# Optimization experiments

Hardware: AMD Instinct MI355X
Metric: run time of the kernel (lower is better)

Reference implementation:

```python
import jax, jax.numpy as jnp
import numpy as np
import math

N, E = 50000, 800000
NFEAT, HID, NCLASS = 512, 96, 64
NUM_LAYERS = 8
ALPHA, THETA = 0.1, 0.5


def setup_inputs() -> dict:
    key = jax.random.key(0)
    ks = jax.random.split(key, 8)
    x = jax.random.normal(ks[0], (N, NFEAT), dtype=jnp.float32)
    # dense_to_sparse(adj_t) -> edge_index; weights are discarded by the module,
    # so propagation uses unit edge weights. We generate the edge list directly.
    edge_index = jax.random.randint(ks[1], (2, E), 0, N, dtype=jnp.int32)
    s_in = 1.0 / math.sqrt(NFEAT)
    s_hid = 1.0 / math.sqrt(HID)
    W_in = jax.random.uniform(ks[2], (NFEAT, HID), jnp.float32, -s_in, s_in)
    b_in = jax.random.uniform(ks[3], (HID,), jnp.float32, -s_in, s_in)
    conv_W = jax.random.uniform(ks[4], (NUM_LAYERS, HID, HID), jnp.float32, -s_hid, s_hid)
    W_out = jax.random.uniform(ks[5], (HID, NCLASS), jnp.float32, -s_hid, s_hid)
    b_out = jax.random.uniform(ks[6], (NCLASS,), jnp.float32, -s_hid, s_hid)
    return {"x": x, "edge_index": edge_index, "W_in": W_in, "b_in": b_in,
            "conv_W": conv_W, "W_out": W_out, "b_out": b_out}


def reference(x, edge_index, W_in, b_in, conv_W, W_out, b_out):
    # Eval mode: dropout is identity.
    src, dst = edge_index[0], edge_index[1]
    h = jax.nn.relu(x @ W_in + b_in)          # [N, HID]
    x0 = h
    for layer in range(NUM_LAYERS):
        beta = math.log(THETA / (layer + 1) + 1.0)
        # sparse propagation: out[i] = sum over edges (j -> i) of h[j]
        agg = jax.ops.segment_sum(h[src], dst, num_segments=N)   # [N, HID]
        hc = (1.0 - ALPHA) * agg + ALPHA * x0                    # initial residual
        h = jax.nn.relu((1.0 - beta) * hc + beta * (hc @ conv_W[layer]))
    out = h @ W_out + b_out                   # [N, NCLASS]
    return jax.nn.log_softmax(out, axis=-1)
```

## Files before the change

### kernel.cpp

```cpp
#include <hip/hip_runtime.h>
#include <math.h>

#define N_NODES 50000
#define N_EDGES 800000
#define NFEAT   512
#define HID     96
#define NCLASS  64
#define NUM_LAYERS 8
#define ALPHA   0.1f
#define NSB     49
#define NBB     196

typedef __attribute__((ext_vector_type(8))) short short8;
typedef __attribute__((ext_vector_type(4))) float f32x4;

__device__ __forceinline__ unsigned short f2bf(float f) {
    unsigned int u = __float_as_uint(f);
    unsigned int r = u + 0x7FFF + ((u >> 16) & 1);
    return (unsigned short)(r >> 16);
}
__device__ __forceinline__ float bflo(unsigned int u) { return __uint_as_float(u << 16); }
__device__ __forceinline__ float bfhi(unsigned int u) { return __uint_as_float(u & 0xFFFF0000u); }
__device__ __forceinline__ float bf2f(short s) {
    return __uint_as_float(((unsigned int)(unsigned short)s) << 16);
}

__global__ void hist_kernel(const int* __restrict__ dst, int* __restrict__ deg) {
    int e = blockIdx.x * blockDim.x + threadIdx.x;
    if (e < N_EDGES) atomicAdd(&deg[dst[e]], 1);
}

__global__ void scan1_kernel(const int* __restrict__ deg, int* __restrict__ row_start,
                             int* __restrict__ blk_sum) {
    __shared__ int sd[1024];
    int t = threadIdx.x;
    int i = blockIdx.x * 1024 + t;
    int v = (i < N_NODES) ? ((deg[i] + 3) & ~3) : 0;
    sd[t] = v;
    __syncthreads();
    for (int off = 1; off < 1024; off <<= 1) {
        int tv = (t >= off) ? sd[t - off] : 0;
        __syncthreads();
        sd[t] += tv;
        __syncthreads();
    }
    if (i < N_NODES) row_start[i] = sd[t] - v;
    if (t == 1023) blk_sum[blockIdx.x] = sd[1023];
}

__global__ void scan2_kernel(const int* __restrict__ blk_sum, int* __restrict__ blk_off) {
    if (threadIdx.x == 0) {
        int acc = 0;
        for (int b = 0; b < NSB; b++) { blk_off[b] = acc; acc += blk_sum[b]; }
    }
}

__global__ void scan3_kernel(int* __restrict__ row_start, const int* __restrict__ blk_off) {
    int i = blockIdx.x * 1024 + threadIdx.x;
    if (i < N_NODES) row_start[i] += blk_off[blockIdx.x];
}

__global__ void fill_kernel(const int* __restrict__ src, const int* __restrict__ dst,
                            const int* __restrict__ row_start, int* __restrict__ cursor,
                            int* __restrict__ csr_src) {
    int e = blockIdx.x * blockDim.x + threadIdx.x;
    if (e < N_EDGES) {
        int d = dst[e];
        int pos = row_start[d] + atomicAdd(&cursor[d], 1);
        csr_src[pos] = src[e];
    }
}

__global__ void pad_kernel(const int* __restrict__ deg, const int* __restrict__ row_start,
                           int* __restrict__ csr_src) {
    int n = blockIdx.x * blockDim.x + threadIdx.x;
    if (n < N_NODES) {
        int d = deg[n], pd = (d + 3) & ~3, rs = row_start[n];
        for (int p = d; p < pd; p++) csr_src[rs + p] = N_NODES;
    }
}

__global__ __launch_bounds__(256) void bin_hist2_kernel(
        const int* __restrict__ deg, int* __restrict__ node_rank,
        int* __restrict__ blk_bin_cnt) {
    __shared__ int lh[64];
    int t = threadIdx.x;
    if (t < 64) lh[t] = 0;
    __syncthreads();
    int n = blockIdx.x * 256 + t;
    if (n < N_NODES) {
        int nq = (deg[n] + 3) >> 2; if (nq > 63) nq = 63;
        node_rank[n] = atomicAdd(&lh[nq], 1);
    }
    __syncthreads();
    if (t < 64) blk_bin_cnt[blockIdx.x * 64 + t] = lh[t];
}

__global__ void bin_offsets_kernel(const int* __restrict__ blk_bin_cnt,
                                   int* __restrict__ blk_bin_off,
                                   int* __restrict__ bin_base) {
    __shared__ int tot[64];
    int b = threadIdx.x;
    int acc = 0;
    for (int blk = 0; blk < NBB; blk++) {
        blk_bin_off[blk * 64 + b] = acc;
        acc += blk_bin_cnt[blk * 64 + b];
    }
    tot[b] = acc;
    __syncthreads();
    if (b == 0) {
        int a = 0;
        for (int i = 63; i >= 0; i--) { bin_base[i] = a; a += tot[i]; }
    }
}

__global__ __launch_bounds__(256) void bin_place_kernel(
        const int* __restrict__ deg, const int* __restrict__ node_rank,
        const int* __restrict__ blk_bin_off, const int* __restrict__ bin_base,
        int* __restrict__ perm) {
    int n = blockIdx.x * 256 + threadIdx.x;
    if (n < N_NODES) {
        int nq = (deg[n] + 3) >> 2; if (nq > 63) nq = 63;
        perm[bin_base[nq] + blk_bin_off[blockIdx.x * 64 + nq] + node_rank[n]] = n;
    }
}

__global__ void zero_dummy_kernel(short* __restrict__ h0, short* __restrict__ hb,
                                  short* __restrict__ hc) {
    int t = threadIdx.x;
    if (t < HID) {
        h0[(size_t)N_NODES * HID + t] = 0;
        hb[(size_t)N_NODES * HID + t] = 0;
        hc[(size_t)N_NODES * HID + t] = 0;
    }
}

__global__ void convert_win_kernel(const float* __restrict__ W, short* __restrict__ Wt) {
    int n = blockIdx.x;
    int k = threadIdx.x;
    Wt[(size_t)n * NFEAT + k] = (short)f2bf(W[(size_t)k * HID + n]);
}

__global__ void convert_wout_kernel(const float* __restrict__ W, short* __restrict__ Wt) {
    int n = blockIdx.x;
    int k = threadIdx.x;
    Wt[(size_t)n * HID + k] = (short)f2bf(W[(size_t)k * NCLASS + n]);
}

__global__ void convert_wconv_kernel(const float* __restrict__ W, short* __restrict__ Wc) {
    int n = blockIdx.x;
    int l = blockIdx.y;
    int k = threadIdx.x;
    Wc[(size_t)l * HID * HID + (size_t)n * HID + k] =
        (short)f2bf(W[(size_t)l * HID * HID + (size_t)k * HID + n]);
}

__global__ __launch_bounds__(256) void gemm_in_kernel(
        const float* __restrict__ x, const short* __restrict__ Wt,
        const float* __restrict__ b, short* __restrict__ h0) {
    int tid  = threadIdx.x;
    int wave = tid >> 6, lane = tid & 63;
    int quad = lane >> 4, l16 = lane & 15;
    int row0 = blockIdx.x * 64 + wave * 16;
    int arow = row0 + l16; if (arow >= N_NODES) arow = N_NODES - 1;
    const float* xrow = &x[(size_t)arow * NFEAT];
    const short* wrow = &Wt[(size_t)l16 * NFEAT + quad * 8];

    f32x4 acc[6];
#pragma unroll
    for (int n = 0; n < 6; n++) acc[n] = (f32x4){0.f, 0.f, 0.f, 0.f};

#pragma unroll
    for (int k0 = 0; k0 < NFEAT; k0 += 32) {
        float4 v0 = *(const float4*)&xrow[k0 + quad * 8];
        float4 v1 = *(const float4*)&xrow[k0 + quad * 8 + 4];
        union { short8 s; uint4 u; } af;
        af.u.x = (unsigned)f2bf(v0.x) | ((unsigned)f2bf(v0.y) << 16);
        af.u.y = (unsigned)f2bf(v0.z) | ((unsigned)f2bf(v0.w) << 16);
        af.u.z = (unsigned)f2bf(v1.x) | ((unsigned)f2bf(v1.y) << 16);
        af.u.w = (unsigned)f2bf(v1.z) | ((unsigned)f2bf(v1.w) << 16);
#pragma unroll
        for (int n = 0; n < 6; n++) {
            short8 bfrag = *(const short8*)&wrow[(size_t)n * 16 * NFEAT + k0];
            acc[n] = __builtin_amdgcn_mfma_f32_16x16x32_bf16(af.s, bfrag, acc[n], 0, 0, 0);
        }
    }
#pragma unroll
    for (int n = 0; n < 6; n++) {
        int col = n * 16 + l16;
        float bias = b[col];
#pragma unroll
        for (int r = 0; r < 4; r++) {
            int grow = row0 + quad * 4 + r;
            if (grow < N_NODES) {
                float v = acc[n][r] + bias;
                v = v > 0.f ? v : 0.f;
                h0[(size_t)grow * HID + col] = (short)f2bf(v);
            }
        }
    }
}

__global__ __launch_bounds__(384) void layer_kernel(
        const short* __restrict__ h_in, const short* __restrict__ x0bf,
        const int* __restrict__ row_start, const int* __restrict__ deg,
        const int* __restrict__ csr_src, const int* __restrict__ perm,
        const short* __restrict__ Wc, float beta, short* __restrict__ h_out) {
    __shared__ short As[32][104];
    __shared__ int   snode[32];
    int tid = threadIdx.x;
    int tx = tid % 12;
    int ty = tid / 12;
    int idx = blockIdx.x * 32 + ty;
    bool valid = idx < N_NODES;
    int node = valid ? perm[idx] : (N_NODES - 1);
    if (tx == 0) snode[ty] = valid ? node : -1;

    int s = row_start[node];
    int d = deg[node];
    int nq = (d + 3) >> 2;
    const int4* c4 = (const int4*)(csr_src + s);
    float acc[8];
#pragma unroll
    for (int j = 0; j < 8; j++) acc[j] = 0.f;
    for (int i = 0; i < nq; i++) {
        int4 idxv = c4[i];
        uint4 a0 = *(const uint4*)&h_in[(size_t)idxv.x * HID + tx * 8];
        uint4 a1 = *(const uint4*)&h_in[(size_t)idxv.y * HID + tx * 8];
        uint4 a2 = *(const uint4*)&h_in[(size_t)idxv.z * HID + tx * 8];
        uint4 a3 = *(const uint4*)&h_in[(size_t)idxv.w * HID + tx * 8];
        acc[0] += bflo(a0.x) + bflo(a1.x) + bflo(a2.x) + bflo(a3.x);
        acc[1] += bfhi(a0.x) + bfhi(a1.x) + bfhi(a2.x) + bfhi(a3.x);
        acc[2] += bflo(a0.y) + bflo(a1.y) + bflo(a2.y) + bflo(a3.y);
        acc[3] += bfhi(a0.y) + bfhi(a1.y) + bfhi(a2.y) + bfhi(a3.y);
        acc[4] += bflo(a0.z) + bflo(a1.z) + bflo(a2.z) + bflo(a3.z);
        acc[5] += bfhi(a0.z) + bfhi(a1.z) + bfhi(a2.z) + bfhi(a3.z);
        acc[6] += bflo(a0.w) + bflo(a1.w) + bflo(a2.w) + bflo(a3.w);
        acc[7] += bfhi(a0.w) + bfhi(a1.w) + bfhi(a2.w) + bfhi(a3.w);
    }
    uint4 xq = *(const uint4*)&x0bf[(size_t)node * HID + tx * 8];
    float hc[8];
    hc[0] = (1.f - ALPHA) * acc[0] + ALPHA * bflo(xq.x);
    hc[1] = (1.f - ALPHA) * acc[1] + ALPHA * bfhi(xq.x);
    hc[2] = (1.f - ALPHA) * acc[2] + ALPHA * bflo(xq.y);
    hc[3] = (1.f - ALPHA) * acc[3] + ALPHA * bfhi(xq.y);
    hc[4] = (1.f - ALPHA) * acc[4] + ALPHA * bflo(xq.z);
    hc[5] = (1.f - ALPHA) * acc[5] + ALPHA * bfhi(xq.z);
    hc[6] = (1.f - ALPHA) * acc[6] + ALPHA * bflo(xq.w);
    hc[7] = (1.f - ALPHA) * acc[7] + ALPHA * bfhi(xq.w);
    {
        uint4 pk;
        pk.x = (unsigned)f2bf(hc[0]) | ((unsigned)f2bf(hc[1]) << 16);
        pk.y = (unsigned)f2bf(hc[2]) | ((unsigned)f2bf(hc[3]) << 16);
        pk.z = (unsigned)f2bf(hc[4]) | ((unsigned)f2bf(hc[5]) << 16);
        pk.w = (unsigned)f2bf(hc[6]) | ((unsigned)f2bf(hc[7]) << 16);
        *(uint4*)&As[ty][tx * 8] = pk;
    }
    __syncthreads();

    int wave = tid >> 6, lane = tid & 63;
    int quad = lane >> 4, l16 = lane & 15;
    int rt = wave & 1;
    int ct0 = (wave >> 1) * 2, ct1 = ct0 + 1;

    f32x4 g0 = (f32x4){0.f,0.f,0.f,0.f}, g1 = (f32x4){0.f,0.f,0.f,0.f};
#pragma unroll
    for (int ks = 0; ks < 3; ks++) {
        short8 afrag = *(const short8*)&As[rt * 16 + l16][ks * 32 + quad * 8];
        short8 b0 = *(const short8*)&Wc[(size_t)(ct0 * 16 + l16) * HID + ks * 32 + quad * 8];
        short8 b1 = *(const short8*)&Wc[(size_t)(ct1 * 16 + l16) * HID + ks * 32 + quad * 8];
        g0 = __builtin_amdgcn_mfma_f32_16x16x32_bf16(afrag, b0, g0, 0, 0, 0);
        g1 = __builtin_amdgcn_mfma_f32_16x16x32_bf16(afrag, b1, g1, 0, 0, 0);
    }
    float ob = 1.0f - beta;
#pragma unroll
    for (int r = 0; r < 4; r++) {
        int lrow = rt * 16 + quad * 4 + r;
        int nd = snode[lrow];
        if (nd >= 0) {
            int c0 = ct0 * 16 + l16;
            int c1 = ct1 * 16 + l16;
            float v0 = ob * bf2f(As[lrow][c0]) + beta * g0[r];
            float v1 = ob * bf2f(As[lrow][c1]) + beta * g1[r];
            v0 = v0 > 0.f ? v0 : 0.f;
            v1 = v1 > 0.f ? v1 : 0.f;
            h_out[(size_t)nd * HID + c0] = (short)f2bf(v0);
            h_out[(size_t)nd * HID + c1] = (short)f2bf(v1);
        }
    }
}

__global__ __launch_bounds__(256) void out_kernel(
        const short* __restrict__ h_bf, const short* __restrict__ Wt,
        const float* __restrict__ b, float* __restrict__ out) {
    int tid = threadIdx.x;
    int wave = tid >> 6, lane = tid & 63;
    int quad = lane >> 4, l16 = lane & 15;
    int row0 = blockIdx.x * 64 + wave * 16;

    f32x4 acc[4];
#pragma unroll
    for (int n = 0; n < 4; n++) acc[n] = (f32x4){0.f, 0.f, 0.f, 0.f};

    int arow = row0 + l16; if (arow > N_NODES) arow = N_NODES;
#pragma unroll
    for (int ks = 0; ks < 3; ks++) {
        short8 afrag = *(const short8*)&h_bf[(size_t)arow * HID + ks * 32 + quad * 8];
#pragma unroll
        for (int n = 0; n < 4; n++) {
            short8 bfrag = *(const short8*)&Wt[(size_t)(n * 16 + l16) * HID + ks * 32 + quad * 8];
            acc[n] = __builtin_amdgcn_mfma_f32_16x16x32_bf16(afrag, bfrag, acc[n], 0, 0, 0);
        }
    }
#pragma unroll
    for (int n = 0; n < 4; n++) {
        float bias = b[n * 16 + l16];
#pragma unroll
        for (int r = 0; r < 4; r++) acc[n][r] += bias;
    }
#pragma unroll
    for (int r = 0; r < 4; r++) {
        float m = acc[0][r];
        m = fmaxf(m, acc[1][r]); m = fmaxf(m, acc[2][r]); m = fmaxf(m, acc[3][r]);
#pragma unroll
        for (int off = 1; off < 16; off <<= 1) m = fmaxf(m, __shfl_xor(m, off));
        float s = __expf(acc[0][r] - m) + __expf(acc[1][r] - m)
                + __expf(acc[2][r] - m) + __expf(acc[3][r] - m);
#pragma unroll
        for (int off = 1; off < 16; off <<= 1) s += __shfl_xor(s, off);
        float lse = m + __logf(s);
        int grow = row0 + quad * 4 + r;
        if (grow < N_NODES) {
#pragma unroll
            for (int n = 0; n < 4; n++)
                out[(size_t)grow * NCLASS + n * 16 + l16] = acc[n][r] - lse;
        }
    }
}

extern "C" void kernel_launch(void* const* d_in, const int* in_sizes, int n_in,
                              void* d_out, int out_size, void* d_ws, size_t ws_size,
                              hipStream_t stream) {
    const float* x      = (const float*)d_in[0];
    const int*   ei     = (const int*)d_in[1];
    const int*   srcp   = ei;
    const int*   dstp   = ei + N_EDGES;
    const float* W_in   = (const float*)d_in[2];
    const float* b_in   = (const float*)d_in[3];
    const float* conv_W = (const float*)d_in[4];
    const float* W_out  = (const float*)d_in[5];
    const float* b_out  = (const float*)d_in[6];
    float* out = (float*)d_out;

    short* h0  = (short*)d_ws;
    short* h_b = h0  + (size_t)(N_NODES + 1) * HID;
    short* h_c = h_b + (size_t)(N_NODES + 1) * HID;
    short* Wt_in  = h_c + (size_t)(N_NODES + 1) * HID;
    short* Wt_out = Wt_in + (size_t)HID * NFEAT;
    short* Wc     = Wt_out + (size_t)NCLASS * HID;
    int* deg        = (int*)(Wc + (size_t)NUM_LAYERS * HID * HID);
    int* row_start  = deg + N_NODES;
    int* cursor     = row_start + N_NODES;
    int* blk_sum    = cursor + N_NODES;
    int* blk_off    = blk_sum + 64;
    int* bin_base   = blk_off + 64;
    int* node_rank  = bin_base + 64;
    int* perm       = node_rank + N_NODES;
    int* blk_bin_cnt= perm + N_NODES;
    int* blk_bin_off= blk_bin_cnt + NBB * 64;
    int* csr_src    = blk_bin_off + NBB * 64;

    hipMemsetAsync(deg,    0, N_NODES * sizeof(int), stream);
    hipMemsetAsync(cursor, 0, N_NODES * sizeof(int), stream);
    hist_kernel<<<(N_EDGES + 255) / 256, 256, 0, stream>>>(dstp, deg);
    scan1_kernel<<<NSB, 1024, 0, stream>>>(deg, row_start, blk_sum);
    scan2_kernel<<<1, 64, 0, stream>>>(blk_sum, blk_off);
    scan3_kernel<<<NSB, 1024, 0, stream>>>(row_start, blk_off);
    fill_kernel<<<(N_EDGES + 255) / 256, 256, 0, stream>>>(srcp, dstp, row_start, cursor, csr_src);
    pad_kernel<<<(N_NODES + 255) / 256, 256, 0, stream>>>(deg, row_start, csr_src);
    bin_hist2_kernel<<<NBB, 256, 0, stream>>>(deg, node_rank, blk_bin_cnt);
    bin_offsets_kernel<<<1, 64, 0, stream>>>(blk_bin_cnt, blk_bin_off, bin_base);
    bin_place_kernel<<<NBB, 256, 0, stream>>>(deg, node_rank, blk_bin_off, bin_base, perm);

    convert_win_kernel<<<HID, NFEAT, 0, stream>>>(W_in, Wt_in);
    convert_wout_kernel<<<NCLASS, HID, 0, stream>>>(W_out, Wt_out);
    convert_wconv_kernel<<<dim3(HID, NUM_LAYERS), HID, 0, stream>>>(conv_W, Wc);
    gemm_in_kernel<<<(N_NODES + 63) / 64, 256, 0, stream>>>(x, Wt_in, b_in, h0);
    zero_dummy_kernel<<<1, 128, 0, stream>>>(h0, h_b, h_c);

    short* cur = h0;
    short* nxt = h_b;
    for (int l = 0; l < NUM_LAYERS; l++) {
        float beta = logf(0.5f / (float)(l + 1) + 1.0f);
        layer_kernel<<<(N_NODES + 31) / 32, 384, 0, stream>>>(
            cur, h0, row_start, deg, csr_src, perm, Wc + (size_t)l * HID * HID, beta, nxt);
        cur = nxt;
        nxt = (cur == h_b) ? h_c : h_b;
    }

    out_kernel<<<(N_NODES + 63) / 64, 256, 0, stream>>>(cur, Wt_out, b_out, out);
}
```

Measured before the change: 563.3 us.

## Pad hidden row stride to 128, unroll gather by 8, split input GEMM columns

Hidden-state buffers use a 128-element row stride so each gathered row is 256-byte aligned, aiming to reduce cache lines touched per random neighbor fetch. CSR rows are padded to multiples of 8 and the aggregation loop gathers 8 neighbors per iteration for more memory-level parallelism. The input GEMM is split into two column halves across a second grid dimension, raising parallelism but reading x twice. Padding also raises memory footprint and wasted padded-edge work for low-degree nodes.

```diff
diff --git a/kernel.cpp b/kernel.cpp
--- a/kernel.cpp
+++ b/kernel.cpp
@@ -5,6 +5,7 @@
 #define N_EDGES 800000
 #define NFEAT   512
 #define HID     96
+#define HSTR    128
 #define NCLASS  64
 #define NUM_LAYERS 8
 #define ALPHA   0.1f
@@ -35,7 +36,7 @@
     __shared__ int sd[1024];
     int t = threadIdx.x;
     int i = blockIdx.x * 1024 + t;
-    int v = (i < N_NODES) ? ((deg[i] + 3) & ~3) : 0;
+    int v = (i < N_NODES) ? ((deg[i] + 7) & ~7) : 0;
     sd[t] = v;
     __syncthreads();
     for (int off = 1; off < 1024; off <<= 1) {
@@ -75,7 +76,7 @@
                            int* __restrict__ csr_src) {
     int n = blockIdx.x * blockDim.x + threadIdx.x;
     if (n < N_NODES) {
-        int d = deg[n], pd = (d + 3) & ~3, rs = row_start[n];
+        int d = deg[n], pd = (d + 7) & ~7, rs = row_start[n];
         for (int p = d; p < pd; p++) csr_src[rs + p] = N_NODES;
     }
 }
@@ -89,7 +90,7 @@
     __syncthreads();
     int n = blockIdx.x * 256 + t;
     if (n < N_NODES) {
-        int nq = (deg[n] + 3) >> 2; if (nq > 63) nq = 63;
+        int nq = (deg[n] + 7) >> 3; if (nq > 63) nq = 63;
         node_rank[n] = atomicAdd(&lh[nq], 1);
     }
     __syncthreads();
@@ -120,7 +121,7 @@
         int* __restrict__ perm) {
     int n = blockIdx.x * 256 + threadIdx.x;
     if (n < N_NODES) {
-        int nq = (deg[n] + 3) >> 2; if (nq > 63) nq = 63;
+        int nq = (deg[n] + 7) >> 3; if (nq > 63) nq = 63;
         perm[bin_base[nq] + blk_bin_off[blockIdx.x * 64 + nq] + node_rank[n]] = n;
     }
 }
@@ -128,10 +129,10 @@
 __global__ void zero_dummy_kernel(short* __restrict__ h0, short* __restrict__ hb,
                                   short* __restrict__ hc) {
     int t = threadIdx.x;
-    if (t < HID) {
-        h0[(size_t)N_NODES * HID + t] = 0;
-        hb[(size_t)N_NODES * HID + t] = 0;
-        hc[(size_t)N_NODES * HID + t] = 0;
+    if (t < HSTR) {
+        h0[(size_t)N_NODES * HSTR + t] = 0;
+        hb[(size_t)N_NODES * HSTR + t] = 0;
+        hc[(size_t)N_NODES * HSTR + t] = 0;
     }
 }
 
@@ -162,13 +163,14 @@
     int wave = tid >> 6, lane = tid & 63;
     int quad = lane >> 4, l16 = lane & 15;
     int row0 = blockIdx.x * 64 + wave * 16;
+    int ch   = blockIdx.y;
     int arow = row0 + l16; if (arow >= N_NODES) arow = N_NODES - 1;
     const float* xrow = &x[(size_t)arow * NFEAT];
-    const short* wrow = &Wt[(size_t)l16 * NFEAT + quad * 8];
-
-    f32x4 acc[6];
-#pragma unroll
-    for (int n = 0; n < 6; n++) acc[n] = (f32x4){0.f, 0.f, 0.f, 0.f};
+    const short* wrow = &Wt[(size_t)(ch * 48 + l16) * NFEAT + quad * 8];
+
+    f32x4 acc[3];
+#pragma unroll
+    for (int n = 0; n < 3; n++) acc[n] = (f32x4){0.f, 0.f, 0.f, 0.f};
 
 #pragma unroll
     for (int k0 = 0; k0 < NFEAT; k0 += 32) {
@@ -180,14 +182,14 @@
         af.u.z = (unsigned)f2bf(v1.x) | ((unsigned)f2bf(v1.y) << 16);
         af.u.w = (unsigned)f2bf(v1.z) | ((unsigned)f2bf(v1.w) << 16);
 #pragma unroll
-        for (int n = 0; n < 6; n++) {
+        for (int n = 0; n < 3; n++) {
             short8 bfrag = *(const short8*)&wrow[(size_t)n * 16 * NFEAT + k0];
             acc[n] = __builtin_amdgcn_mfma_f32_16x16x32_bf16(af.s, bfrag, acc[n], 0, 0, 0);
         }
     }
 #pragma unroll
-    for (int n = 0; n < 6; n++) {
-        int col = n * 16 + l16;
+    for (int n = 0; n < 3; n++) {
+        int col = ch * 48 + n * 16 + l16;
         float bias = b[col];
 #pragma unroll
         for (int r = 0; r < 4; r++) {
@@ -195,7 +197,7 @@
             if (grow < N_NODES) {
                 float v = acc[n][r] + bias;
                 v = v > 0.f ? v : 0.f;
-                h0[(size_t)grow * HID + col] = (short)f2bf(v);
+                h0[(size_t)grow * HSTR + col] = (short)f2bf(v);
             }
         }
     }
@@ -218,27 +220,40 @@
 
     int s = row_start[node];
     int d = deg[node];
-    int nq = (d + 3) >> 2;
+    int n8 = (d + 7) >> 3;
     const int4* c4 = (const int4*)(csr_src + s);
     float acc[8];
 #pragma unroll
     for (int j = 0; j < 8; j++) acc[j] = 0.f;
-    for (int i = 0; i < nq; i++) {
-        int4 idxv = c4[i];
-        uint4 a0 = *(const uint4*)&h_in[(size_t)idxv.x * HID + tx * 8];
-        uint4 a1 = *(const uint4*)&h_in[(size_t)idxv.y * HID + tx * 8];
-        uint4 a2 = *(const uint4*)&h_in[(size_t)idxv.z * HID + tx * 8];
-        uint4 a3 = *(const uint4*)&h_in[(size_t)idxv.w * HID + tx * 8];
-        acc[0] += bflo(a0.x) + bflo(a1.x) + bflo(a2.x) + bflo(a3.x);
-        acc[1] += bfhi(a0.x) + bfhi(a1.x) + bfhi(a2.x) + bfhi(a3.x);
-        acc[2] += bflo(a0.y) + bflo(a1.y) + bflo(a2.y) + bflo(a3.y);
-        acc[3] += bfhi(a0.y) + bfhi(a1.y) + bfhi(a2.y) + bfhi(a3.y);
-        acc[4] += bflo(a0.z) + bflo(a1.z) + bflo(a2.z) + bflo(a3.z);
-        acc[5] += bfhi(a0.z) + bfhi(a1.z) + bfhi(a2.z) + bfhi(a3.z);
-        acc[6] += bflo(a0.w) + bflo(a1.w) + bflo(a2.w) + bflo(a3.w);
-        acc[7] += bfhi(a0.w) + bfhi(a1.w) + bfhi(a2.w) + bfhi(a3.w);
-    }
-    uint4 xq = *(const uint4*)&x0bf[(size_t)node * HID + tx * 8];
+    for (int i = 0; i < n8; i++) {
+        int4 ia = c4[2 * i];
+        int4 ib = c4[2 * i + 1];
+        uint4 a0 = *(const uint4*)&h_in[(size_t)ia.x * HSTR + tx * 8];
+        uint4 a1 = *(const uint4*)&h_in[(size_t)ia.y * HSTR + tx * 8];
+        uint4 a2 = *(const uint4*)&h_in[(size_t)ia.z * HSTR + tx * 8];
+        uint4 a3 = *(const uint4*)&h_in[(size_t)ia.w * HSTR + tx * 8];
+        uint4 a4 = *(const uint4*)&h_in[(size_t)ib.x * HSTR + tx * 8];
+        uint4 a5 = *(const uint4*)&h_in[(size_t)ib.y * HSTR + tx * 8];
+        uint4 a6 = *(const uint4*)&h_in[(size_t)ib.z * HSTR + tx * 8];
+        uint4 a7 = *(const uint4*)&h_in[(size_t)ib.w * HSTR + tx * 8];
+        acc[0] += (bflo(a0.x) + bflo(a1.x)) + (bflo(a2.x) + bflo(a3.x))
+                + (bflo(a4.x) + bflo(a5.x)) + (bflo(a6.x) + bflo(a7.x));
+        acc[1] += (bfhi(a0.x) + bfhi(a1.x)) + (bfhi(a2.x) + bfhi(a3.x))
+                + (bfhi(a4.x) + bfhi(a5.x)) + (bfhi(a6.x) + bfhi(a7.x));
+        acc[2] += (bflo(a0.y) + bflo(a1.y)) + (bflo(a2.y) + bflo(a3.y))
+                + (bflo(a4.y) + bflo(a5.y)) + (bflo(a6.y) + bflo(a7.y));
+        acc[3] += (bfhi(a0.y) + bfhi(a1.y)) + (bfhi(a2.y) + bfhi(a3.y))
+                + (bfhi(a4.y) + bfhi(a5.y)) + (bfhi(a6.y) + bfhi(a7.y));
+        acc[4] += (bflo(a0.z) + bflo(a1.z)) + (bflo(a2.z) + bflo(a3.z))
+                + (bflo(a4.z) + bflo(a5.z)) + (bflo(a6.z) + bflo(a7.z));
+        acc[5] += (bfhi(a0.z) + bfhi(a1.z)) + (bfhi(a2.z) + bfhi(a3.z))
+                + (bfhi(a4.z) + bfhi(a5.z)) + (bfhi(a6.z) + bfhi(a7.z));
+        acc[6] += (bflo(a0.w) + bflo(a1.w)) + (bflo(a2.w) + bflo(a3.w))
+                + (bflo(a4.w) + bflo(a5.w)) + (bflo(a6.w) + bflo(a7.w));
+        acc[7] += (bfhi(a0.w) + bfhi(a1.w)) + (bfhi(a2.w) + bfhi(a3.w))
+                + (bfhi(a4.w) + bfhi(a5.w)) + (bfhi(a6.w) + bfhi(a7.w));
+    }
+    uint4 xq = *(const uint4*)&x0bf[(size_t)node * HSTR + tx * 8];
     float hc[8];
     hc[0] = (1.f - ALPHA) * acc[0] + ALPHA * bflo(xq.x);
     hc[1] = (1.f - ALPHA) * acc[1] + ALPHA * bfhi(xq.x);
@@ -284,8 +299,8 @@
             float v1 = ob * bf2f(As[lrow][c1]) + beta * g1[r];
             v0 = v0 > 0.f ? v0 : 0.f;
             v1 = v1 > 0.f ? v1 : 0.f;
-            h_out[(size_t)nd * HID + c0] = (short)f2bf(v0);
-            h_out[(size_t)nd * HID + c1] = (short)f2bf(v1);
+            h_out[(size_t)nd * HSTR + c0] = (short)f2bf(v0);
+            h_out[(size_t)nd * HSTR + c1] = (short)f2bf(v1);
         }
     }
 }
@@ -305,7 +320,7 @@
     int arow = row0 + l16; if (arow > N_NODES) arow = N_NODES;
 #pragma unroll
     for (int ks = 0; ks < 3; ks++) {
-        short8 afrag = *(const short8*)&h_bf[(size_t)arow * HID + ks * 32 + quad * 8];
+        short8 afrag = *(const short8*)&h_bf[(size_t)arow * HSTR + ks * 32 + quad * 8];
 #pragma unroll
         for (int n = 0; n < 4; n++) {
             short8 bfrag = *(const short8*)&Wt[(size_t)(n * 16 + l16) * HID + ks * 32 + quad * 8];
@@ -353,9 +368,9 @@
     float* out = (float*)d_out;
 
     short* h0  = (short*)d_ws;
-    short* h_b = h0  + (size_t)(N_NODES + 1) * HID;
-    short* h_c = h_b + (size_t)(N_NODES + 1) * HID;
-    short* Wt_in  = h_c + (size_t)(N_NODES + 1) * HID;
+    short* h_b = h0  + (size_t)(N_NODES + 1) * HSTR;
+    short* h_c = h_b + (size_t)(N_NODES + 1) * HSTR;
+    short* Wt_in  = h_c + (size_t)(N_NODES + 1) * HSTR;
     short* Wt_out = Wt_in + (size_t)HID * NFEAT;
     short* Wc     = Wt_out + (size_t)NCLASS * HID;
     int* deg        = (int*)(Wc + (size_t)NUM_LAYERS * HID * HID);
@@ -385,7 +400,7 @@
     convert_win_kernel<<<HID, NFEAT, 0, stream>>>(W_in, Wt_in);
     convert_wout_kernel<<<NCLASS, HID, 0, stream>>>(W_out, Wt_out);
     convert_wconv_kernel<<<dim3(HID, NUM_LAYERS), HID, 0, stream>>>(conv_W, Wc);
-    gemm_in_kernel<<<(N_NODES + 63) / 64, 256, 0, stream>>>(x, Wt_in, b_in, h0);
+    gemm_in_kernel<<<dim3((N_NODES + 63) / 64, 2), 256, 0, stream>>>(x, Wt_in, b_in, h0);
     zero_dummy_kernel<<<1, 128, 0, stream>>>(h0, h_b, h_c);
 
     short* cur = h0;
```

Result: slower. 585.2 us (+3.9%).
